# Performance work log

Hardware: AMD Instinct MI355X
Metric: run time of the kernel (lower is better)

Reference implementation:

```python
import jax, jax.numpy as jnp
import numpy as np

B, S = 256, 256          # batch of collocation points, pseudo-sequence length
L, D, H = 4, 512, 8      # retnet layers (hardcoded 4), d_model, heads
HD = D // H              # head size 64
HV = 2 * HD              # double_v_dim -> v head size 128
V = H * HV               # v_dim 1024
FFN, DH, DOUT = 128, 512, 1


def _ln(x, w, b, eps=1e-5):
    mu = jnp.mean(x, -1, keepdims=True)
    var = jnp.var(x, -1, keepdims=True)
    return (x - mu) * jax.lax.rsqrt(var + eps) * w + b


def _rotate_every_two(x):
    x1, x2 = x[..., ::2], x[..., 1::2]
    return jnp.stack([-x2, x1], axis=-1).reshape(x.shape)


def _xpos_tables(seq, hd):
    half = hd // 2
    sv = (jnp.arange(0, hd, 2, dtype=jnp.float32) + 0.4 * hd) / (1.4 * hd)
    power = jnp.arange(seq, dtype=jnp.float32) / 512.0  # xpos scale_base = 512
    scale = sv[None, :] ** power[:, None]               # [S, half]
    inv_freq = 1.0 / (10000.0 ** (jnp.arange(half, dtype=jnp.float32) / half))
    ang = jnp.arange(seq, dtype=jnp.float32)[:, None] * inv_freq[None, :]
    return jnp.sin(ang), jnp.cos(ang), scale


def _apply_xpos(x, sin, cos, scale):
    # duplicate_interleave(sin*scale) == repeat each column twice
    s = jnp.repeat(sin * scale, 2, axis=-1)  # [S, hd]
    c = jnp.repeat(cos * scale, 2, axis=-1)
    return x * c + _rotate_every_two(x) * s


def setup_inputs() -> dict:
    key = jax.random.key(0)
    ks = iter(jax.random.split(key, 40))
    def nrm(shape, fan_in):
        return jax.random.normal(next(ks), shape, jnp.float32) / np.float32(np.sqrt(fan_in))
    return {
        'x': jax.random.uniform(next(ks), (B, S, 1), jnp.float32),
        't': jax.random.uniform(next(ks), (B, S, 1), jnp.float32),
        'emb_W': nrm((2, D), 2), 'emb_b': jnp.zeros((D,), jnp.float32),
        'ln1_w': jnp.ones((L, D), jnp.float32), 'ln1_b': jnp.zeros((L, D), jnp.float32),
        'ln2_w': jnp.ones((L, D), jnp.float32), 'ln2_b': jnp.zeros((L, D), jnp.float32),
        'WQ': nrm((L, H, D, HD), D), 'WK': nrm((L, H, D, HD), D), 'WV': nrm((L, H, D, HV), D),
        'WG': nrm((L, D, V), D), 'WO': nrm((L, V, D), V),
        'gn_w': jnp.ones((L, V), jnp.float32), 'gn_b': jnp.zeros((L, V), jnp.float32),
        'f1_W': nrm((L, D, FFN), D), 'f1_b': jnp.zeros((L, FFN), jnp.float32),
        'f2_W': nrm((L, FFN, D), FFN), 'f2_b': jnp.zeros((L, D), jnp.float32),
        'h1_W': nrm((D, DH), D), 'h1_b': jnp.zeros((DH,), jnp.float32),
        'wave_w': jnp.ones((2, 2), jnp.float32),
        'h2_W': nrm((DH, DH), DH), 'h2_b': jnp.zeros((DH,), jnp.float32),
        'h3_W': nrm((DH, DOUT), DH), 'h3_b': jnp.zeros((DOUT,), jnp.float32),
    }


def reference(x, t, emb_W, emb_b, ln1_w, ln1_b, ln2_w, ln2_b, WQ, WK, WV, WG, WO,
              gn_w, gn_b, f1_W, f1_b, f2_W, f2_b, h1_W, h1_b, wave_w, h2_W, h2_b,
              h3_W, h3_b):
    src = jnp.concatenate([x, t], -1) @ emb_W + emb_b  # [B,S,D]
    sin, cos, scale = _xpos_tables(S, HD)
    # per-head decay gammas, multi-scale retention
    gammas = (1.0 - jnp.exp(jnp.linspace(np.log(1 / 32), np.log(1 / 512), H))).astype(jnp.float32)
    n = jnp.arange(S)
    diff = n[:, None] - n[None, :]
    Dm = jnp.where(diff >= 0, gammas[:, None, None] ** jnp.maximum(diff, 0), 0.0)  # [H,S,S]
    X = src
    for l in range(L):
        Xn = _ln(X, ln1_w[l], ln1_b[l])
        Q = jnp.einsum('bsd,hde->bhse', Xn, WQ[l])
        K = jnp.einsum('bsd,hde->bhse', Xn, WK[l])
        Vv = jnp.einsum('bsd,hdv->bhsv', Xn, WV[l])  # [B,H,S,HV]
        Q = _apply_xpos(Q, sin, cos, scale)
        K = _apply_xpos(K, sin, cos, 1.0 / scale)  # downscale=True
        A = jnp.einsum('bhse,bhme->bhsm', Q, K) * Dm  # decayed retention scores
        Y = jnp.einsum('bhsm,bhmv->bhsv', A, Vv)
        Y = jnp.transpose(Y, (0, 2, 1, 3))  # [B,S,H,HV]; GroupNorm group = head
        mu = jnp.mean(Y, -1, keepdims=True)
        var = jnp.var(Y, -1, keepdims=True)
        Y = (Y - mu) * jax.lax.rsqrt(var + 1e-5)
        Y = Y.reshape(X.shape[0], S, V) * gn_w[l] + gn_b[l]
        G = Xn @ WG[l]
        G = G * jax.nn.sigmoid(G)  # swish gate
        Yr = (G * Y) @ WO[l] + X   # residual 1
        Yn = _ln(Yr, ln2_w[l], ln2_b[l])
        X = (jax.nn.gelu(Yn @ f1_W[l] + f1_b[l], approximate=False) @ f2_W[l] + f2_b[l]) + Yr
    # WaveAct MLP head
    h = X @ h1_W + h1_b
    h = wave_w[0, 0] * jnp.sin(h) + wave_w[0, 1] * jnp.cos(h)
    h = h @ h2_W + h2_b
    h = wave_w[1, 0] * jnp.sin(h) + wave_w[1, 1] * jnp.cos(h)
    return h @ h3_W + h3_b
```

## Files before the change

kernel.cpp:

```cpp
#include <hip/hip_runtime.h>
#include <cstdint>
#include <cstddef>

#define DEV static __device__ __forceinline__

typedef short bf16x8 __attribute__((ext_vector_type(8)));
typedef float f32x4 __attribute__((ext_vector_type(4)));
typedef unsigned short u16;

DEV float wredf(float v) {
  v += __shfl_xor(v, 32, 64); v += __shfl_xor(v, 16, 64);
  v += __shfl_xor(v, 8, 64);  v += __shfl_xor(v, 4, 64);
  v += __shfl_xor(v, 2, 64);  v += __shfl_xor(v, 1, 64);
  return v;
}

DEV void ld4(float* d, const float* p) {
  float4 t = *(const float4*)p;
  d[0] = t.x; d[1] = t.y; d[2] = t.z; d[3] = t.w;
}
DEV void st4(float* p, const float* s) {
  *(float4*)p = make_float4(s[0], s[1], s[2], s[3]);
}

DEV unsigned int bfh16(float v) {
  unsigned int u = __float_as_uint(v);
  return (u + 0x7FFFu + ((u >> 16) & 1u)) >> 16;
}
DEV uint2 splitpk(float a, float b) {
  unsigned int ha = bfh16(a), hb = bfh16(b);
  float la = a - __uint_as_float(ha << 16);
  float lb = b - __uint_as_float(hb << 16);
  return make_uint2(ha | (hb << 16), bfh16(la) | (bfh16(lb) << 16));
}

DEV size_t swz_idx(int row, int col, int ld) {
  return (size_t)row * ld + (col & ~31) +
         ((((col >> 3) & 3) ^ ((row >> 1) & 3)) << 3) + (col & 7);
}

DEV void gload_lds16(const void* g, void* l) {
  __builtin_amdgcn_global_load_lds(
      (const __attribute__((address_space(1))) unsigned int*)g,
      (__attribute__((address_space(3))) unsigned int*)l, 16, 0, 0);
}

__global__ __launch_bounds__(256)
void tab_kernel(float* __restrict__ rtab) {
  const int idx = blockIdx.x * 256 + threadIdx.x;
  if (idx < 16384) {
    const int tk = idx >> 13;
    const int e = idx & 8191;
    const int s = e >> 5, i = e & 31;
    const float sv = (2.0f * i + 25.6f) / 89.6f;
    const float sc = powf(sv, (float)s / 512.0f);
    const float invf = powf(10000.0f, -(float)i / 32.0f);
    const float ang = (float)s * invf;
    const float f = tk ? 1.0f / sc : sc;
    rtab[tk * 16384 + e * 2]     = cosf(ang) * f;
    rtab[tk * 16384 + e * 2 + 1] = sinf(ang) * f;
  } else if (idx < 20480) {
    const int e = idx - 16384;
    const int tk = e >> 11;
    const int he = e & 2047;
    const int h = he >> 8, s = he & 255;
    const float l32 = logf(1.0f / 32.0f), l512 = logf(1.0f / 512.0f);
    const float gamma = 1.0f - expf(l32 + (float)h * (l512 - l32) / 7.0f);
    const float g = powf(gamma, (float)s);
    rtab[32768 + e] = tk ? 1.0f / g : g;
  }
}

__global__ __launch_bounds__(256)
void embed_kernel(const float* __restrict__ x, const float* __restrict__ t,
                  const float* __restrict__ W, const float* __restrict__ eb,
                  float* __restrict__ X) {
  const int gid = blockIdx.x * 256 + threadIdx.x;
  const int row = gid >> 6, d = (gid & 63) * 8;
  const float xv = x[row], tv = t[row];
  #pragma unroll
  for (int j = 0; j < 8; j++)
    X[(size_t)row * 512 + d + j] =
        xv * W[d + j] + tv * W[512 + d + j] + eb[d + j];
}

__global__ __launch_bounds__(256)
void ln_split(const float* __restrict__ X, const float* __restrict__ w,
              const float* __restrict__ bb, u16* __restrict__ hi,
              u16* __restrict__ lo) {
  const int row = blockIdx.x * 4 + (threadIdx.x >> 6);
  const int lane = threadIdx.x & 63;
  const float* xp = X + (size_t)row * 512 + lane * 8;
  float4 a0 = *(const float4*)xp;
  float4 a1 = *(const float4*)(xp + 4);
  float v[8] = {a0.x, a0.y, a0.z, a0.w, a1.x, a1.y, a1.z, a1.w};
  float s = 0.f, sq = 0.f;
  #pragma unroll
  for (int j = 0; j < 8; j++) { s += v[j]; sq += v[j] * v[j]; }
  s = wredf(s); sq = wredf(sq);
  const float mean = s * (1.f / 512.f);
  const float var = fmaxf(sq * (1.f / 512.f) - mean * mean, 0.f);
  const float inv = rsqrtf(var + 1e-5f);
  const float* wp = w + lane * 8;
  const float* bp = bb + lane * 8;
  float o[8];
  #pragma unroll
  for (int j = 0; j < 8; j++)
    o[j] = (v[j] - mean) * inv * wp[j] + bp[j];
  uint2 p0 = splitpk(o[0], o[1]), p1 = splitpk(o[2], o[3]);
  uint2 p2 = splitpk(o[4], o[5]), p3 = splitpk(o[6], o[7]);
  const size_t off = swz_idx(row, lane * 8, 512);
  *(int4*)(hi + off) = make_int4(p0.x, p1.x, p2.x, p3.x);
  *(int4*)(lo + off) = make_int4(p0.y, p1.y, p2.y, p3.y);
}

__global__ __launch_bounds__(256)
void split_kernel(const float* __restrict__ X, u16* __restrict__ hi,
                  u16* __restrict__ lo) {
  const int row = blockIdx.x * 4 + (threadIdx.x >> 6);
  const int lane = threadIdx.x & 63;
  const float* xp = X + (size_t)row * 512 + lane * 8;
  float v[8];
  ld4(v, xp); ld4(v + 4, xp + 4);
  uint2 p0 = splitpk(v[0], v[1]), p1 = splitpk(v[2], v[3]);
  uint2 p2 = splitpk(v[4], v[5]), p3 = splitpk(v[6], v[7]);
  const size_t off = swz_idx(row, lane * 8, 512);
  *(int4*)(hi + off) = make_int4(p0.x, p1.x, p2.x, p3.x);
  *(int4*)(lo + off) = make_int4(p0.y, p1.y, p2.y, p3.y);
}

__global__ __launch_bounds__(256)
void attn_fused(const float* __restrict__ QKV, u16* __restrict__ GYh,
                u16* __restrict__ GYl, const float* __restrict__ gw,
                const float* __restrict__ gb, const float* __restrict__ rtab) {
  __shared__ float Qs[64][68];
  __shared__ float Ks[64][68];
  __shared__ float At[64][68];
  const int h = blockIdx.y;
  const int r0 = blockIdx.x * 64;
  const int b = r0 >> 8;
  const int s0 = r0 & 255;
  const int st = s0 >> 6;
  const int tid = threadIdx.x;
  const int ty = tid >> 4, tx = tid & 15;
  const int rr = tid >> 2, e0 = (tid & 3) * 16;

  {
    const int s = (r0 + rr) & 255;
    const float gq = rtab[32768 + h * 256 + s];
    const float* qp = QKV + (size_t)(r0 + rr) * 3072 + h * 64 + e0;
    const float* rt = rtab + ((size_t)s * 32 + (e0 >> 1)) * 2;
    #pragma unroll
    for (int j = 0; j < 8; j++) {
      const float c = rt[2 * j] * gq, sn = rt[2 * j + 1] * gq;
      const float v0 = qp[2 * j], v1 = qp[2 * j + 1];
      Qs[e0 + 2 * j][rr]     = v0 * c - v1 * sn;
      Qs[e0 + 2 * j + 1][rr] = v1 * c + v0 * sn;
    }
  }

  float acc2[4][8];
  #pragma unroll
  for (int i = 0; i < 4; i++)
    #pragma unroll
    for (int j = 0; j < 8; j++) acc2[i][j] = 0.f;

  for (int mt = 0; mt <= st; mt++) {
    const int m0 = mt * 64;
    {
      const int m = m0 + rr;
      const float gk = rtab[34816 + h * 256 + m];
      const float* kp = QKV + (size_t)(b * 256 + m) * 3072 + 512 + h * 64 + e0;
      const float* rt = rtab + 16384 + ((size_t)m * 32 + (e0 >> 1)) * 2;
      #pragma unroll
      for (int j = 0; j < 8; j++) {
        const float c = rt[2 * j] * gk, sn = rt[2 * j + 1] * gk;
        const float v0 = kp[2 * j], v1 = kp[2 * j + 1];
        Ks[e0 + 2 * j][rr]     = v0 * c - v1 * sn;
        Ks[e0 + 2 * j + 1][rr] = v1 * c + v0 * sn;
      }
    }
    __syncthreads();
    float a1[4][4];
    #pragma unroll
    for (int i = 0; i < 4; i++)
      #pragma unroll
      for (int j = 0; j < 4; j++) a1[i][j] = 0.f;
    #pragma unroll 4
    for (int e = 0; e < 64; e++) {
      float qa[4], kb[4];
      ld4(qa, &Qs[e][ty * 4]);
      ld4(kb, &Ks[e][tx * 4]);
      #pragma unroll
      for (int i = 0; i < 4; i++)
        #pragma unroll
        for (int j = 0; j < 4; j++)
          a1[i][j] = fmaf(qa[i], kb[j], a1[i][j]);
    }
    #pragma unroll
    for (int i = 0; i < 4; i++)
      #pragma unroll
      for (int j = 0; j < 4; j++) {
        float v = a1[i][j];
        if (mt == st && (m0 + tx * 4 + j) > (s0 + ty * 4 + i)) v = 0.f;
        At[tx * 4 + j][ty * 4 + i] = v;
      }
    __syncthreads();
    const float* vp = QKV + (size_t)(b * 256 + m0) * 3072 + 1024 + h * 128 + tx * 8;
    #pragma unroll 4
    for (int m = 0; m < 64; m++) {
      float av[4], vv[8];
      ld4(av, &At[m][ty * 4]);
      ld4(vv, vp);
      ld4(vv + 4, vp + 4);
      vp += 3072;
      #pragma unroll
      for (int i = 0; i < 4; i++)
        #pragma unroll
        for (int j = 0; j < 8; j++)
          acc2[i][j] = fmaf(av[i], vv[j], acc2[i][j]);
    }
    __syncthreads();
  }

  const int vi = h * 128 + tx * 8;
  float gwv[8], gbv[8];
  ld4(gwv, gw + vi); ld4(gwv + 4, gw + vi + 4);
  ld4(gbv, gb + vi); ld4(gbv + 4, gb + vi + 4);
  #pragma unroll
  for (int i = 0; i < 4; i++) {
    const int row = r0 + ty * 4 + i;
    float s = 0.f, sq = 0.f;
    #pragma unroll
    for (int j = 0; j < 8; j++) { s += acc2[i][j]; sq += acc2[i][j] * acc2[i][j]; }
    #pragma unroll
    for (int msk = 1; msk <= 8; msk <<= 1) {
      s += __shfl_xor(s, msk, 64);
      sq += __shfl_xor(sq, msk, 64);
    }
    const float mean = s * (1.f / 128.f);
    const float var = fmaxf(sq * (1.f / 128.f) - mean * mean, 0.f);
    const float inv = rsqrtf(var + 1e-5f);
    const float* gp = QKV + (size_t)row * 3072 + 2048 + vi;
    float gs[8];
    ld4(gs, gp); ld4(gs + 4, gp + 4);
    float o[8];
    #pragma unroll
    for (int j = 0; j < 8; j++)
      o[j] = ((acc2[i][j] - mean) * inv * gwv[j] + gbv[j]) * gs[j];
    uint2 p0 = splitpk(o[0], o[1]), p1 = splitpk(o[2], o[3]);
    uint2 p2 = splitpk(o[4], o[5]), p3 = splitpk(o[6], o[7]);
    const size_t off = swz_idx(row, vi, 1024);
    *(int4*)(GYh + off) = make_int4(p0.x, p1.x, p2.x, p3.x);
    *(int4*)(GYl + off) = make_int4(p0.y, p1.y, p2.y, p3.y);
  }
}

__global__ __launch_bounds__(256)
void head3_kernel(const float* __restrict__ X, const float* __restrict__ w,
                  const float* __restrict__ b3, float* __restrict__ out) {
  const int row = blockIdx.x * 4 + (threadIdx.x >> 6);
  const int lane = threadIdx.x & 63;
  const float* xp = X + (size_t)row * 512 + lane * 8;
  const float* wp = w + lane * 8;
  float s = 0.f;
  #pragma unroll
  for (int j = 0; j < 8; j++) s += xp[j] * wp[j];
  s = wredf(s);
  if (lane == 0) out[row] = s + b3[0];
}

__global__ __launch_bounds__(256)
void pack_plain(const float* __restrict__ W, u16* __restrict__ hi,
                u16* __restrict__ lo, int N, int kshift) {
  const int idx = blockIdx.x * 256 + threadIdx.x;
  const int K = 1 << kshift;
  const int n = idx >> kshift, k = idx & (K - 1);
  const float v = W[(size_t)k * N + n];
  const unsigned int h = bfh16(v);
  const float l = v - __uint_as_float(h << 16);
  const size_t o = swz_idx(n, k, K);
  hi[o] = (u16)h;
  lo[o] = (u16)bfh16(l);
}

__global__ __launch_bounds__(256)
void pack_qkvg(const float* __restrict__ WQ, const float* __restrict__ WK,
               const float* __restrict__ WV, const float* __restrict__ WG,
               u16* __restrict__ hi, u16* __restrict__ lo) {
  const int idx = blockIdx.x * 256 + threadIdx.x;
  const int c = idx >> 9, k = idx & 511;
  float v;
  if (c < 512)
    v = WQ[((size_t)(c >> 6) * 512 + k) * 64 + (c & 63)];
  else if (c < 1024)
    v = WK[((size_t)((c - 512) >> 6) * 512 + k) * 64 + ((c - 512) & 63)];
  else if (c < 2048)
    v = WV[((size_t)((c - 1024) >> 7) * 512 + k) * 128 + ((c - 1024) & 127)];
  else
    v = WG[(size_t)k * 1024 + (c - 2048)];
  const unsigned int h = bfh16(v);
  const float l = v - __uint_as_float(h << 16);
  const size_t o = swz_idx(c, k, 512);
  hi[o] = (u16)h;
  lo[o] = (u16)bfh16(l);
}

template<int EPI, int OSPLIT>
__global__ __launch_bounds__(256, 2)
void gemm_lds(const u16* __restrict__ Agh, const u16* __restrict__ Agl,
              const u16* __restrict__ Bh, const u16* __restrict__ Bl,
              float* __restrict__ C, u16* __restrict__ Ch, u16* __restrict__ Cl,
              const int N, const int K,
              const float* __restrict__ bias, const float* __restrict__ aux,
              const float* __restrict__ wave2) {
  __shared__ __align__(16) u16 S[2][4][128][32];
  const int tid = threadIdx.x;
  const int lane = tid & 63;
  const int wave = tid >> 6;
  const int wr = (wave >> 1) * 64, wc = (wave & 1) * 64;

  int bx = blockIdx.x, by = blockIdx.y;
  {
    const int gx = gridDim.x, gy = gridDim.y;
    const int nwg = gx * gy;
    if ((nwg & 7) == 0) {
      const int id = by * gx + bx;
      const int q = nwg >> 3;
      const int L = (id & 7) * q + (id >> 3);
      bx = L / gy;
      by = L - bx * gy;
    }
  }
  const int m0 = by * 128, n0 = bx * 128;

  const int fm = lane & 15;
  const int q = lane >> 4;

  const u16* pb;
  if (wave == 0)      pb = Agh + (size_t)m0 * K;
  else if (wave == 1) pb = Agl + (size_t)m0 * K;
  else if (wave == 2) pb = Bh + (size_t)n0 * K;
  else                pb = Bl + (size_t)n0 * K;
  const u16* src0 = pb + (size_t)(lane >> 2) * K + (lane & 3) * 8;

  f32x4 acc[4][4];
  #pragma unroll
  for (int i = 0; i < 4; i++)
    #pragma unroll
    for (int j = 0; j < 4; j++)
      acc[i][j] = (f32x4){0.f, 0.f, 0.f, 0.f};

  {
    u16* dst = &S[0][wave][0][0];
    #pragma unroll
    for (int i = 0; i < 8; i++)
      gload_lds16(src0 + (size_t)(i * 16) * K, dst + i * 512);
  }
  __syncthreads();

  for (int kt = 0; kt < K; kt += 32) {
    const int cur = (kt >> 5) & 1;
    if (kt + 32 < K) {
      u16* dst = &S[cur ^ 1][wave][0][0];
      const u16* s = src0 + kt + 32;
      #pragma unroll
      for (int i = 0; i < 8; i++)
        gload_lds16(s + (size_t)(i * 16) * K, dst + i * 512);
      asm volatile("s_waitcnt vmcnt(8)" ::: "memory");
    } else {
      asm volatile("s_waitcnt vmcnt(0)" ::: "memory");
    }
    __builtin_amdgcn_sched_barrier(0);
    __builtin_amdgcn_s_barrier();
    __builtin_amdgcn_sched_barrier(0);
    __builtin_amdgcn_s_setprio(1);

    bf16x8 avh[4], avl[4];
    #pragma unroll
    for (int mf = 0; mf < 4; mf++) {
      const int m = wr + mf * 16 + fm;
      const int c = (q ^ ((m >> 1) & 3)) * 8;
      avh[mf] = *(const bf16x8*)&S[cur][0][m][c];
      avl[mf] = *(const bf16x8*)&S[cur][1][m][c];
    }
    #pragma unroll
    for (int nf = 0; nf < 4; nf++) {
      const int n = wc + nf * 16 + fm;
      const int c = (q ^ ((n >> 1) & 3)) * 8;
      bf16x8 bh = *(const bf16x8*)&S[cur][2][n][c];
      bf16x8 bl = *(const bf16x8*)&S[cur][3][n][c];
      #pragma unroll
      for (int mf = 0; mf < 4; mf++) {
        acc[mf][nf] = __builtin_amdgcn_mfma_f32_16x16x32_bf16(avh[mf], bh, acc[mf][nf], 0, 0, 0);
        acc[mf][nf] = __builtin_amdgcn_mfma_f32_16x16x32_bf16(avl[mf], bh, acc[mf][nf], 0, 0, 0);
        acc[mf][nf] = __builtin_amdgcn_mfma_f32_16x16x32_bf16(avh[mf], bl, acc[mf][nf], 0, 0, 0);
      }
    }
    __builtin_amdgcn_s_setprio(0);
    __builtin_amdgcn_sched_barrier(0);
    __builtin_amdgcn_s_barrier();
  }

  const int r0 = m0 + wr + (lane >> 4) * 4;
  const int c0 = n0 + wc + fm;
  #pragma unroll
  for (int mf = 0; mf < 4; mf++) {
    #pragma unroll
    for (int nf = 0; nf < 4; nf++) {
      const int col = c0 + nf * 16;
      #pragma unroll
      for (int r = 0; r < 4; r++) {
        const int row = r0 + mf * 16 + r;
        const size_t idx = (size_t)row * N + col;
        float v = acc[mf][nf][r];
        float o;
        if constexpr (EPI == 0) {
          o = v;
        } else if constexpr (EPI == 2) {
          o = v + aux[idx];
        } else if constexpr (EPI == 3) {
          v += bias[col];
          o = 0.5f * v * (1.f + erff(v * 0.70710678118654752f));
        } else if constexpr (EPI == 4) {
          o = v + bias[col] + aux[idx];
        } else if constexpr (EPI == 5) {
          v += bias[col];
          o = wave2[0] * sinf(v) + wave2[1] * cosf(v);
        } else {
          if (col < 2048) o = v;
          else            o = v / (1.f + expf(-v));
        }
        if constexpr (OSPLIT == 0) {
          C[idx] = o;
        } else {
          const size_t sidx = swz_idx(row, col, N);
          const unsigned int hb = bfh16(o);
          Ch[sidx] = (u16)hb;
          Cl[sidx] = (u16)bfh16(o - __uint_as_float(hb << 16));
        }
      }
    }
  }
}


extern "C" void kernel_launch(void* const* d_in, const int* in_sizes, int n_in,
                              void* d_out, int out_size, void* d_ws, size_t ws_size,
                              hipStream_t stream) {
  (void)in_sizes; (void)n_in; (void)out_size;
  const float* x    = (const float*)d_in[0];
  const float* t    = (const float*)d_in[1];
  const float* embW = (const float*)d_in[2];
  const float* embB = (const float*)d_in[3];
  const float* ln1w = (const float*)d_in[4];
  const float* ln1b = (const float*)d_in[5];
  const float* ln2w = (const float*)d_in[6];
  const float* ln2b = (const float*)d_in[7];
  const float* WQ   = (const float*)d_in[8];
  const float* WK   = (const float*)d_in[9];
  const float* WV   = (const float*)d_in[10];
  const float* WG   = (const float*)d_in[11];
  const float* WO   = (const float*)d_in[12];
  const float* gnw  = (const float*)d_in[13];
  const float* gnb  = (const float*)d_in[14];
  const float* f1W  = (const float*)d_in[15];
  const float* f1b  = (const float*)d_in[16];
  const float* f2W  = (const float*)d_in[17];
  const float* f2bp = (const float*)d_in[18];
  const float* h1W  = (const float*)d_in[19];
  const float* h1b  = (const float*)d_in[20];
  const float* wvw  = (const float*)d_in[21];
  const float* h2W  = (const float*)d_in[22];
  const float* h2b  = (const float*)d_in[23];
  const float* h3W  = (const float*)d_in[24];
  const float* h3b  = (const float*)d_in[25];

  u16* P = (u16*)d_ws;
  const size_t SQKVG = 3072 * 512, SWO = 512 * 1024;
  const size_t SF1 = 128 * 512, SF2 = 512 * 128;
  const size_t PERL = 2 * (SQKVG + SWO + SF1 + SF2);
  const size_t HOFF = 4 * PERL;
  const size_t PACK_BYTES = (HOFF + 4 * 512 * 512) * 2;
  const size_t TAB_BYTES = 36864 * 4;

  u16* h1h = P + HOFF;
  u16* h1l = h1h + 512 * 512;
  u16* h2h = h1l + 512 * 512;
  u16* h2l = h2h + 512 * 512;
  float* RT = (float*)((char*)d_ws + PACK_BYTES);

  const dim3 blk(256);

  tab_kernel<<<dim3(80), blk, 0, stream>>>(RT);
  for (int l = 0; l < 4; l++) {
    u16* qkvh = P + l * PERL;
    u16* qkvl = qkvh + SQKVG;
    u16* woh  = qkvl + SQKVG;
    u16* wol  = woh + SWO;
    u16* f1h  = wol + SWO;
    u16* f1l  = f1h + SF1;
    u16* f2h  = f1l + SF1;
    u16* f2l  = f2h + SF2;
    pack_qkvg<<<dim3(SQKVG / 256), blk, 0, stream>>>(
        WQ + (size_t)l * 262144, WK + (size_t)l * 262144,
        WV + (size_t)l * 524288, WG + (size_t)l * 524288, qkvh, qkvl);
    pack_plain<<<dim3(SWO / 256), blk, 0, stream>>>(WO + (size_t)l * 524288, woh, wol, 512, 10);
    pack_plain<<<dim3(SF1 / 256), blk, 0, stream>>>(f1W + (size_t)l * 65536, f1h, f1l, 128, 9);
    pack_plain<<<dim3(SF2 / 256), blk, 0, stream>>>(f2W + (size_t)l * 65536, f2h, f2l, 512, 7);
  }
  pack_plain<<<dim3(1024), blk, 0, stream>>>(h1W, h1h, h1l, 512, 9);
  pack_plain<<<dim3(1024), blk, 0, stream>>>(h2W, h2h, h2l, 512, 9);

  const size_t BASE = PACK_BYTES + TAB_BYTES;
  int NC = 4;
  while (NC < 256) {
    const size_t R = 65536u / NC;
    if (BASE + R * 22528 + 4096 <= ws_size) break;
    NC <<= 1;
  }
  const int R = 65536 / NC;

  float* Xf   = (float*)((char*)d_ws + BASE);
  float* Xn   = Xf  + (size_t)R * 512;
  float* QKVG = Xn  + (size_t)R * 512;
  float* GYb  = QKVG + (size_t)R * 3072;
  float* Yr   = GYb + (size_t)R * 1024;

  u16* Xnh = (u16*)Xn;           u16* Xnl = Xnh + (size_t)R * 512;
  u16* GYh = (u16*)GYb;          u16* GYl = GYh + (size_t)R * 1024;
  u16* midh = (u16*)GYb;         u16* midl = midh + (size_t)R * 128;
  u16* H1h = (u16*)GYb;          u16* H1l = H1h + (size_t)R * 512;

  for (int c = 0; c < NC; c++) {
    const size_t off = (size_t)c * R;
    embed_kernel<<<dim3(R / 4), blk, 0, stream>>>(x + off, t + off, embW, embB, Xf);

    for (int l = 0; l < 4; l++) {
      u16* qkvh = P + l * PERL;
      u16* qkvl = qkvh + SQKVG;
      u16* woh  = qkvl + SQKVG;
      u16* wol  = woh + SWO;
      u16* f1h  = wol + SWO;
      u16* f1l  = f1h + SF1;
      u16* f2h  = f1l + SF1;
      u16* f2l  = f2h + SF2;

      ln_split<<<dim3(R / 4), blk, 0, stream>>>(Xf, ln1w + l * 512, ln1b + l * 512, Xnh, Xnl);
      gemm_lds<6, 0><<<dim3(24, R / 128), blk, 0, stream>>>(
          Xnh, Xnl, qkvh, qkvl, QKVG, nullptr, nullptr,
          3072, 512, nullptr, nullptr, nullptr);
      attn_fused<<<dim3(R / 64, 8), blk, 0, stream>>>(
          QKVG, GYh, GYl, gnw + l * 1024, gnb + l * 1024, RT);
      gemm_lds<2, 0><<<dim3(4, R / 128), blk, 0, stream>>>(
          GYh, GYl, woh, wol, Yr, nullptr, nullptr,
          512, 1024, nullptr, Xf, nullptr);
      ln_split<<<dim3(R / 4), blk, 0, stream>>>(Yr, ln2w + l * 512, ln2b + l * 512, Xnh, Xnl);
      gemm_lds<3, 1><<<dim3(1, R / 128), blk, 0, stream>>>(
          Xnh, Xnl, f1h, f1l, nullptr, midh, midl,
          128, 512, f1b + l * 128, nullptr, nullptr);
      gemm_lds<4, 0><<<dim3(4, R / 128), blk, 0, stream>>>(
          midh, midl, f2h, f2l, Xf, nullptr, nullptr,
          512, 128, f2bp + l * 512, Yr, nullptr);
    }

    split_kernel<<<dim3(R / 4), blk, 0, stream>>>(Xf, Xnh, Xnl);
    gemm_lds<5, 1><<<dim3(4, R / 128), blk, 0, stream>>>(
        Xnh, Xnl, h1h, h1l, nullptr, H1h, H1l,
        512, 512, h1b, nullptr, wvw);
    gemm_lds<5, 0><<<dim3(4, R / 128), blk, 0, stream>>>(
        H1h, H1l, h2h, h2l, Yr, nullptr, nullptr,
        512, 512, h2b, nullptr, wvw + 2);
    head3_kernel<<<dim3(R / 4), blk, 0, stream>>>(
        Yr, h3W, h3b, (float*)d_out + off);
  }
}
```

Baseline: 10.02 ms.

## Rewrite retention attention kernel with split-bf16 MFMA matrix instructions

```diff
diff --git a/kernel.cpp b/kernel.cpp
--- a/kernel.cpp
+++ b/kernel.cpp
@@ -37,6 +37,11 @@
 DEV size_t swz_idx(int row, int col, int ld) {
   return (size_t)row * ld + (col & ~31) +
          ((((col >> 3) & 3) ^ ((row >> 1) & 3)) << 3) + (col & 7);
+}
+
+DEV int lswc(int row, int c) { return row * 64 + ((c ^ (row & 7)) << 3); }
+DEV int lsw16(int row, int m) {
+  return row * 64 + (((m >> 3) ^ (row & 7)) << 3) + (m & 7);
 }
 
 DEV void gload_lds16(const void* g, void* l) {
@@ -130,109 +135,160 @@
 }
 
 __global__ __launch_bounds__(256)
-void attn_fused(const float* __restrict__ QKV, u16* __restrict__ GYh,
-                u16* __restrict__ GYl, const float* __restrict__ gw,
-                const float* __restrict__ gb, const float* __restrict__ rtab) {
-  __shared__ float Qs[64][68];
-  __shared__ float Ks[64][68];
-  __shared__ float At[64][68];
+void attn_mfma(const float* __restrict__ QKV, u16* __restrict__ GYh,
+               u16* __restrict__ GYl, const float* __restrict__ gw,
+               const float* __restrict__ gb, const float* __restrict__ rtab) {
+  __shared__ __align__(16) u16 QsH[64 * 64], QsL[64 * 64];
+  __shared__ __align__(16) u16 KsH[64 * 64], KsL[64 * 64];
+  __shared__ __align__(16) u16 Ph[64 * 64], Pl[64 * 64];
+  __shared__ __align__(16) u16 VtH[128 * 64], VtL[128 * 64];
   const int h = blockIdx.y;
   const int r0 = blockIdx.x * 64;
   const int b = r0 >> 8;
   const int s0 = r0 & 255;
   const int st = s0 >> 6;
   const int tid = threadIdx.x;
-  const int ty = tid >> 4, tx = tid & 15;
-  const int rr = tid >> 2, e0 = (tid & 3) * 16;
+  const int lane = tid & 63;
+  const int w = tid >> 6;
+  const int fr = lane & 15, fq = lane >> 4;
 
   {
+    const int rr = tid >> 2, e0 = (tid & 3) * 16;
     const int s = (r0 + rr) & 255;
     const float gq = rtab[32768 + h * 256 + s];
     const float* qp = QKV + (size_t)(r0 + rr) * 3072 + h * 64 + e0;
     const float* rt = rtab + ((size_t)s * 32 + (e0 >> 1)) * 2;
+    float o[16];
     #pragma unroll
     for (int j = 0; j < 8; j++) {
       const float c = rt[2 * j] * gq, sn = rt[2 * j + 1] * gq;
       const float v0 = qp[2 * j], v1 = qp[2 * j + 1];
-      Qs[e0 + 2 * j][rr]     = v0 * c - v1 * sn;
-      Qs[e0 + 2 * j + 1][rr] = v1 * c + v0 * sn;
-    }
-  }
-
-  float acc2[4][8];
-  #pragma unroll
-  for (int i = 0; i < 4; i++)
-    #pragma unroll
-    for (int j = 0; j < 8; j++) acc2[i][j] = 0.f;
+      o[2 * j]     = v0 * c - v1 * sn;
+      o[2 * j + 1] = v1 * c + v0 * sn;
+    }
+    uint2 qq[8];
+    #pragma unroll
+    for (int i = 0; i < 8; i++) qq[i] = splitpk(o[2 * i], o[2 * i + 1]);
+    const int c0 = e0 >> 3;
+    *(int4*)&QsH[lswc(rr, c0)]     = make_int4(qq[0].x, qq[1].x, qq[2].x, qq[3].x);
+    *(int4*)&QsH[lswc(rr, c0 + 1)] = make_int4(qq[4].x, qq[5].x, qq[6].x, qq[7].x);
+    *(int4*)&QsL[lswc(rr, c0)]     = make_int4(qq[0].y, qq[1].y, qq[2].y, qq[3].y);
+    *(int4*)&QsL[lswc(rr, c0 + 1)] = make_int4(qq[4].y, qq[5].y, qq[6].y, qq[7].y);
+  }
+
+  f32x4 acc[8];
+  #pragma unroll
+  for (int i = 0; i < 8; i++) acc[i] = (f32x4){0.f, 0.f, 0.f, 0.f};
 
   for (int mt = 0; mt <= st; mt++) {
     const int m0 = mt * 64;
+    __syncthreads();
+
     {
+      const int rr = tid >> 2, e0 = (tid & 3) * 16;
       const int m = m0 + rr;
       const float gk = rtab[34816 + h * 256 + m];
       const float* kp = QKV + (size_t)(b * 256 + m) * 3072 + 512 + h * 64 + e0;
       const float* rt = rtab + 16384 + ((size_t)m * 32 + (e0 >> 1)) * 2;
+      float o[16];
       #pragma unroll
       for (int j = 0; j < 8; j++) {
         const float c = rt[2 * j] * gk, sn = rt[2 * j + 1] * gk;
         const float v0 = kp[2 * j], v1 = kp[2 * j + 1];
-        Ks[e0 + 2 * j][rr]     = v0 * c - v1 * sn;
-        Ks[e0 + 2 * j + 1][rr] = v1 * c + v0 * sn;
+        o[2 * j]     = v0 * c - v1 * sn;
+        o[2 * j + 1] = v1 * c + v0 * sn;
       }
+      uint2 kk[8];
+      #pragma unroll
+      for (int i = 0; i < 8; i++) kk[i] = splitpk(o[2 * i], o[2 * i + 1]);
+      const int c0 = e0 >> 3;
+      *(int4*)&KsH[lswc(rr, c0)]     = make_int4(kk[0].x, kk[1].x, kk[2].x, kk[3].x);
+      *(int4*)&KsH[lswc(rr, c0 + 1)] = make_int4(kk[4].x, kk[5].x, kk[6].x, kk[7].x);
+      *(int4*)&KsL[lswc(rr, c0)]     = make_int4(kk[0].y, kk[1].y, kk[2].y, kk[3].y);
+      *(int4*)&KsL[lswc(rr, c0 + 1)] = make_int4(kk[4].y, kk[5].y, kk[6].y, kk[7].y);
+    }
+    {
+      const int vv = tid >> 1;
+      const int mh = (tid & 1) * 32;
+      const float* vp = QKV + (size_t)(b * 256 + m0 + mh) * 3072 + 1024 + h * 128 + vv;
+      float pvv[32];
+      #pragma unroll
+      for (int mm = 0; mm < 32; mm++) pvv[mm] = vp[(size_t)mm * 3072];
+      uint2 qv[16];
+      #pragma unroll
+      for (int i = 0; i < 16; i++) qv[i] = splitpk(pvv[2 * i], pvv[2 * i + 1]);
+      const int cb = mh >> 3;
+      #pragma unroll
+      for (int j = 0; j < 4; j++) {
+        *(int4*)&VtH[lswc(vv, cb + j)] =
+            make_int4(qv[4 * j].x, qv[4 * j + 1].x, qv[4 * j + 2].x, qv[4 * j + 3].x);
+        *(int4*)&VtL[lswc(vv, cb + j)] =
+            make_int4(qv[4 * j].y, qv[4 * j + 1].y, qv[4 * j + 2].y, qv[4 * j + 3].y);
+      }
     }
     __syncthreads();
-    float a1[4][4];
-    #pragma unroll
-    for (int i = 0; i < 4; i++)
-      #pragma unroll
-      for (int j = 0; j < 4; j++) a1[i][j] = 0.f;
-    #pragma unroll 4
-    for (int e = 0; e < 64; e++) {
-      float qa[4], kb[4];
-      ld4(qa, &Qs[e][ty * 4]);
-      ld4(kb, &Ks[e][tx * 4]);
-      #pragma unroll
-      for (int i = 0; i < 4; i++)
-        #pragma unroll
-        for (int j = 0; j < 4; j++)
-          a1[i][j] = fmaf(qa[i], kb[j], a1[i][j]);
-    }
-    #pragma unroll
-    for (int i = 0; i < 4; i++)
-      #pragma unroll
-      for (int j = 0; j < 4; j++) {
-        float v = a1[i][j];
-        if (mt == st && (m0 + tx * 4 + j) > (s0 + ty * 4 + i)) v = 0.f;
-        At[tx * 4 + j][ty * 4 + i] = v;
+
+    f32x4 sa[4];
+    #pragma unroll
+    for (int i = 0; i < 4; i++) sa[i] = (f32x4){0.f, 0.f, 0.f, 0.f};
+    #pragma unroll
+    for (int kt = 0; kt < 2; kt++) {
+      const int ck = fq + kt * 4;
+      bf16x8 ah = *(const bf16x8*)&QsH[lswc(w * 16 + fr, ck)];
+      bf16x8 al = *(const bf16x8*)&QsL[lswc(w * 16 + fr, ck)];
+      #pragma unroll
+      for (int mf = 0; mf < 4; mf++) {
+        bf16x8 bh = *(const bf16x8*)&KsH[lswc(mf * 16 + fr, ck)];
+        bf16x8 bl = *(const bf16x8*)&KsL[lswc(mf * 16 + fr, ck)];
+        sa[mf] = __builtin_amdgcn_mfma_f32_16x16x32_bf16(ah, bh, sa[mf], 0, 0, 0);
+        sa[mf] = __builtin_amdgcn_mfma_f32_16x16x32_bf16(al, bh, sa[mf], 0, 0, 0);
+        sa[mf] = __builtin_amdgcn_mfma_f32_16x16x32_bf16(ah, bl, sa[mf], 0, 0, 0);
       }
+    }
+    const bool diag = (mt == st);
+    #pragma unroll
+    for (int mf = 0; mf < 4; mf++) {
+      const int ml = mf * 16 + fr;
+      #pragma unroll
+      for (int r = 0; r < 4; r++) {
+        float v = sa[mf][r];
+        const int sl = w * 16 + fq * 4 + r;
+        if (diag && ml > sl) v = 0.f;
+        const unsigned hb = bfh16(v);
+        const int pi = lsw16(sl, ml);
+        Ph[pi] = (u16)hb;
+        Pl[pi] = (u16)bfh16(v - __uint_as_float(hb << 16));
+      }
+    }
     __syncthreads();
-    const float* vp = QKV + (size_t)(b * 256 + m0) * 3072 + 1024 + h * 128 + tx * 8;
-    #pragma unroll 4
-    for (int m = 0; m < 64; m++) {
-      float av[4], vv[8];
-      ld4(av, &At[m][ty * 4]);
-      ld4(vv, vp);
-      ld4(vv + 4, vp + 4);
-      vp += 3072;
-      #pragma unroll
-      for (int i = 0; i < 4; i++)
-        #pragma unroll
-        for (int j = 0; j < 8; j++)
-          acc2[i][j] = fmaf(av[i], vv[j], acc2[i][j]);
-    }
-    __syncthreads();
-  }
-
-  const int vi = h * 128 + tx * 8;
-  float gwv[8], gbv[8];
-  ld4(gwv, gw + vi); ld4(gwv + 4, gw + vi + 4);
-  ld4(gbv, gb + vi); ld4(gbv + 4, gb + vi + 4);
-  #pragma unroll
-  for (int i = 0; i < 4; i++) {
-    const int row = r0 + ty * 4 + i;
+
+    #pragma unroll
+    for (int kt = 0; kt < 2; kt++) {
+      const int ck = fq + kt * 4;
+      bf16x8 ph = *(const bf16x8*)&Ph[lswc(w * 16 + fr, ck)];
+      bf16x8 pl = *(const bf16x8*)&Pl[lswc(w * 16 + fr, ck)];
+      #pragma unroll
+      for (int vf = 0; vf < 8; vf++) {
+        bf16x8 vh = *(const bf16x8*)&VtH[lswc(vf * 16 + fr, ck)];
+        bf16x8 vl = *(const bf16x8*)&VtL[lswc(vf * 16 + fr, ck)];
+        acc[vf] = __builtin_amdgcn_mfma_f32_16x16x32_bf16(ph, vh, acc[vf], 0, 0, 0);
+        acc[vf] = __builtin_amdgcn_mfma_f32_16x16x32_bf16(pl, vh, acc[vf], 0, 0, 0);
+        acc[vf] = __builtin_amdgcn_mfma_f32_16x16x32_bf16(ph, vl, acc[vf], 0, 0, 0);
+      }
+    }
+  }
+
+  const int vi0 = h * 128;
+  #pragma unroll
+  for (int r = 0; r < 4; r++) {
+    const int row = r0 + w * 16 + fq * 4 + r;
+    float vals[8];
     float s = 0.f, sq = 0.f;
     #pragma unroll
-    for (int j = 0; j < 8; j++) { s += acc2[i][j]; sq += acc2[i][j] * acc2[i][j]; }
+    for (int vf = 0; vf < 8; vf++) {
+      vals[vf] = acc[vf][r];
+      s += vals[vf]; sq += vals[vf] * vals[vf];
+    }
     #pragma unroll
     for (int msk = 1; msk <= 8; msk <<= 1) {
       s += __shfl_xor(s, msk, 64);
@@ -241,18 +297,16 @@
     const float mean = s * (1.f / 128.f);
     const float var = fmaxf(sq * (1.f / 128.f) - mean * mean, 0.f);
     const float inv = rsqrtf(var + 1e-5f);
-    const float* gp = QKV + (size_t)row * 3072 + 2048 + vi;
-    float gs[8];
-    ld4(gs, gp); ld4(gs + 4, gp + 4);
-    float o[8];
-    #pragma unroll
-    for (int j = 0; j < 8; j++)
-      o[j] = ((acc2[i][j] - mean) * inv * gwv[j] + gbv[j]) * gs[j];
-    uint2 p0 = splitpk(o[0], o[1]), p1 = splitpk(o[2], o[3]);
-    uint2 p2 = splitpk(o[4], o[5]), p3 = splitpk(o[6], o[7]);
-    const size_t off = swz_idx(row, vi, 1024);
-    *(int4*)(GYh + off) = make_int4(p0.x, p1.x, p2.x, p3.x);
-    *(int4*)(GYl + off) = make_int4(p0.y, p1.y, p2.y, p3.y);
+    const float* gp = QKV + (size_t)row * 3072 + 2048 + vi0;
+    #pragma unroll
+    for (int vf = 0; vf < 8; vf++) {
+      const int vc = vf * 16 + fr;
+      const float o = ((vals[vf] - mean) * inv * gw[vi0 + vc] + gb[vi0 + vc]) * gp[vc];
+      const size_t off = swz_idx(row, vi0 + vc, 1024);
+      const unsigned hb = bfh16(o);
+      GYh[off] = (u16)hb;
+      GYl[off] = (u16)bfh16(o - __uint_as_float(hb << 16));
+    }
   }
 }
 
@@ -550,7 +604,7 @@
       gemm_lds<6, 0><<<dim3(24, R / 128), blk, 0, stream>>>(
           Xnh, Xnl, qkvh, qkvl, QKVG, nullptr, nullptr,
           3072, 512, nullptr, nullptr, nullptr);
-      attn_fused<<<dim3(R / 64, 8), blk, 0, stream>>>(
+      attn_mfma<<<dim3(R / 64, 8), blk, 0, stream>>>(
           QKVG, GYh, GYl, gnw + l * 1024, gnb + l * 1024, RT);
       gemm_lds<2, 0><<<dim3(4, R / 128), blk, 0, stream>>>(
           GYh, GYl, woh, wol, Yr, nullptr, nullptr,
```

New measurement: 8.846 ms. 1.13x faster.
